# Performance work log

Measured on AMD Instinct MI355X. Metric: run time of the kernel, lower is better.

The kernel has to match this reference:

```python
import jax, jax.numpy as jnp
import numpy as np

B, T, C = 2, 2048, 1024
H, D = 16, 64          # n_heads, head_dim
E, K, HD = 8, 2, 1536  # num_experts, active_experts, expert hidden (int(1.5*C))
EPS = 1e-6


def setup_inputs() -> dict:
    key = jax.random.key(0)
    ks = jax.random.split(key, 13)
    s = 0.02
    return {
        "x": jax.random.normal(ks[0], (B, T, C), jnp.float32),
        "rope_cos": jax.random.uniform(ks[1], (T, D), jnp.float32),
        "rope_sin": jax.random.uniform(ks[2], (T, D), jnp.float32),
        "attn_norm_w": jnp.ones((C,), jnp.float32),
        "q_w": jax.random.normal(ks[3], (C, C), jnp.float32) * s,
        "k_w": jax.random.normal(ks[4], (C, C), jnp.float32) * s,
        "v_w": jax.random.normal(ks[5], (C, C), jnp.float32) * s,
        "o_w": jax.random.normal(ks[6], (C, C), jnp.float32) * s,
        "ffn_norm_w": jnp.ones((C,), jnp.float32),
        "router_w": jax.random.normal(ks[7], (E, C), jnp.float32) * s,
        "w1": jax.random.normal(ks[8], (E, HD, C), jnp.float32) * s,
        "w2": jax.random.normal(ks[9], (E, C, HD), jnp.float32) * s,
        "w3": jax.random.normal(ks[10], (E, HD, C), jnp.float32) * s,
    }


def rmsnorm(x, w):
    var = jnp.mean(x * x, axis=-1, keepdims=True)
    return w * x * jax.lax.rsqrt(var + EPS)


def apply_rope(x, cos, sin):
    # x: [B, T, H, D]; cos/sin: [T, D]
    cos = cos[None, :, None, :]
    sin = sin[None, :, None, :]
    d = x.shape[-1] // 2
    x1, x2 = x[..., :d], x[..., d:]
    rotated = jnp.concatenate([-x2, x1], axis=-1)
    return x * cos + rotated * sin


def reference(x, rope_cos, rope_sin, attn_norm_w, q_w, k_w, v_w, o_w,
              ffn_norm_w, router_w, w1, w2, w3):
    b, t, c = x.shape
    h = rmsnorm(x, attn_norm_w)
    q = (h @ q_w.T).reshape(b, t, H, D)
    k = (h @ k_w.T).reshape(b, t, H, D)
    v = (h @ v_w.T).reshape(b, t, H, D)
    q = apply_rope(q, rope_cos[:t], rope_sin[:t]).transpose(0, 2, 1, 3)  # [B,H,T,D]
    k = apply_rope(k, rope_cos[:t], rope_sin[:t]).transpose(0, 2, 1, 3)
    v = v.transpose(0, 2, 1, 3)
    scores = jnp.einsum('bhqd,bhkd->bhqk', q, k) / jnp.sqrt(jnp.asarray(D, q.dtype))
    causal = jnp.tril(jnp.ones((t, t), bool))
    scores = jnp.where(causal, scores, -jnp.inf)
    attn = jax.nn.softmax(scores, axis=-1)
    y = jnp.einsum('bhqk,bhkd->bhqd', attn, v)
    y = y.transpose(0, 2, 1, 3).reshape(b, t, c)
    x = x + y @ o_w.T

    # Sparse MoE (top-K routing, per-expert SwiGLU, weighted combine)
    hn = rmsnorm(x, ffn_norm_w)
    flat = hn.reshape(-1, c)                                # [N, C]
    logits = flat @ router_w.T                              # [N, E]
    wk, idx = jax.lax.top_k(logits, K)                      # [N, K]
    wk = jax.nn.softmax(wk, axis=-1)
    # combined per-expert gate: [N, E] (zero for unrouted experts)
    gate = jnp.sum((idx[..., None] == jnp.arange(E)) * wk[..., None], axis=1)
    out = jnp.zeros_like(flat)
    for e in range(E):
        g = jax.nn.silu(flat @ w1[e].T) * (flat @ w3[e].T)  # [N, HD]
        out = out + gate[:, e:e + 1] * (g @ w2[e].T)
    return x + out.reshape(b, t, c)
```

## Files before the change

### kernel.cpp

```cpp
#include <hip/hip_runtime.h>
#include <hip/hip_bf16.h>
#include <math.h>

#define Bq 2
#define Tq 2048
#define Cq 1024
#define Hq 16
#define Dq 64
#define Eq 8
#define HDq 1536
#define NTOK (Bq*Tq)

typedef unsigned short u16;
typedef _Float16 f16;
typedef __bf16 bf16x8 __attribute__((ext_vector_type(8)));
typedef _Float16 f16x8 __attribute__((ext_vector_type(8)));
typedef float f32x4v __attribute__((ext_vector_type(4)));

#define MB(x) ((size_t)(x) * 262144)

__device__ __forceinline__ float silu_f(float a) {
    return a / (1.0f + __expf(-a));
}
__device__ __forceinline__ u16 f2bf(float f) {
    union { float f; unsigned u; } a; a.f = f;
    unsigned r = a.u + 0x7fffu + ((a.u >> 16) & 1u);
    return (u16)(r >> 16);
}
__device__ __forceinline__ u16 f16bits(f16 h) {
    union { f16 f; u16 u; } a; a.f = h; return a.u;
}

__device__ __forceinline__ void stage16(const void* g, void* l) {
    __builtin_amdgcn_global_load_lds(
        (const __attribute__((address_space(1))) unsigned int*)g,
        (__attribute__((address_space(3))) unsigned int*)l, 16, 0, 0);
}

__global__ __launch_bounds__(256) void rmsnorm_split_k(const float* __restrict__ x,
                                                       const float* __restrict__ w,
                                                       u16* __restrict__ hh,
                                                       u16* __restrict__ hl) {
    int row = blockIdx.x;
    int tid = threadIdx.x;
    const float* xr = x + (size_t)row * Cq;
    float4 v = *(const float4*)(xr + tid * 4);
    float ss = v.x*v.x + v.y*v.y + v.z*v.z + v.w*v.w;
    #pragma unroll
    for (int off = 32; off; off >>= 1) ss += __shfl_xor(ss, off);
    __shared__ float red[4];
    if ((tid & 63) == 0) red[tid >> 6] = ss;
    __syncthreads();
    float tot = red[0] + red[1] + red[2] + red[3];
    float scale = rsqrtf(tot * (1.0f / (float)Cq) + 1e-6f);
    float4 wv = *(const float4*)(w + tid * 4);
    float o[4] = { v.x*wv.x*scale, v.y*wv.y*scale, v.z*wv.z*scale, v.w*wv.w*scale };
    ushort4 oh, ol;
    u16* ph = (u16*)&oh; u16* pl = (u16*)&ol;
    #pragma unroll
    for (int i = 0; i < 4; i++) {
        f16 hi = (f16)o[i]; f16 lo = (f16)(o[i] - (float)hi);
        ph[i] = f16bits(hi); pl[i] = f16bits(lo);
    }
    *(ushort4*)(hh + (size_t)row * Cq + tid * 4) = oh;
    *(ushort4*)(hl + (size_t)row * Cq + tid * 4) = ol;
}

__global__ __launch_bounds__(256) void rmsnorm2_k(const float* __restrict__ x,
                                                  const float* __restrict__ w,
                                                  float* __restrict__ hn,
                                                  u16* __restrict__ hnb) {
    int row = blockIdx.x;
    int tid = threadIdx.x;
    const float* xr = x + (size_t)row * Cq;
    float4 v = *(const float4*)(xr + tid * 4);
    float ss = v.x*v.x + v.y*v.y + v.z*v.z + v.w*v.w;
    #pragma unroll
    for (int off = 32; off; off >>= 1) ss += __shfl_xor(ss, off);
    __shared__ float red[4];
    if ((tid & 63) == 0) red[tid >> 6] = ss;
    __syncthreads();
    float tot = red[0] + red[1] + red[2] + red[3];
    float scale = rsqrtf(tot * (1.0f / (float)Cq) + 1e-6f);
    float4 wv = *(const float4*)(w + tid * 4);
    float4 o = make_float4(v.x*wv.x*scale, v.y*wv.y*scale, v.z*wv.z*scale, v.w*wv.w*scale);
    *(float4*)(hn + (size_t)row * Cq + tid * 4) = o;
    ushort4 ob = make_ushort4(f2bf(o.x), f2bf(o.y), f2bf(o.z), f2bf(o.w));
    *(ushort4*)(hnb + (size_t)row * Cq + tid * 4) = ob;
}

__global__ __launch_bounds__(256) void wconv_k(const float* __restrict__ w1,
                                               const float* __restrict__ w3,
                                               const float* __restrict__ w2,
                                               u16* __restrict__ w1b,
                                               u16* __restrict__ w3b,
                                               u16* __restrict__ w2b) {
    int a = blockIdx.y;
    const float* src = (a == 0) ? w1 : ((a == 1) ? w3 : w2);
    u16* dst = (a == 0) ? w1b : ((a == 1) ? w3b : w2b);
    size_t i = ((size_t)blockIdx.x * 256 + threadIdx.x) * 8;
    float4 f0 = *(const float4*)(src + i);
    float4 f1 = *(const float4*)(src + i + 4);
    ushort4 o0 = make_ushort4(f2bf(f0.x), f2bf(f0.y), f2bf(f0.z), f2bf(f0.w));
    ushort4 o1 = make_ushort4(f2bf(f1.x), f2bf(f1.y), f2bf(f1.z), f2bf(f1.w));
    *(ushort4*)(dst + i)     = o0;
    *(ushort4*)(dst + i + 4) = o1;
}

__global__ __launch_bounds__(256) void wsplit_k(const float* __restrict__ qw,
                                                const float* __restrict__ kw,
                                                const float* __restrict__ vw,
                                                const float* __restrict__ ow,
                                                u16* __restrict__ qhp, u16* __restrict__ qlp,
                                                u16* __restrict__ khp, u16* __restrict__ klp,
                                                u16* __restrict__ vhp, u16* __restrict__ vlp,
                                                u16* __restrict__ ohp, u16* __restrict__ olp) {
    int a = blockIdx.y;
    const float* src = (a == 0) ? qw : ((a == 1) ? kw : ((a == 2) ? vw : ow));
    u16* dh = (a == 0) ? qhp : ((a == 1) ? khp : ((a == 2) ? vhp : ohp));
    u16* dl = (a == 0) ? qlp : ((a == 1) ? klp : ((a == 2) ? vlp : olp));
    size_t i = ((size_t)blockIdx.x * 256 + threadIdx.x) * 8;
    float f[8];
    *(float4*)&f[0] = *(const float4*)(src + i);
    *(float4*)&f[4] = *(const float4*)(src + i + 4);
    u16 oh[8], ol[8];
    #pragma unroll
    for (int j = 0; j < 8; j++) {
        f16 hi = (f16)f[j]; f16 lo = (f16)(f[j] - (float)hi);
        oh[j] = f16bits(hi); ol[j] = f16bits(lo);
    }
    *(uint4*)(dh + i) = *(uint4*)oh;
    *(uint4*)(dl + i) = *(uint4*)ol;
}

__global__ __launch_bounds__(256, 3) void gemm_fused(const u16* __restrict__ Ahg,
                                                     const u16* __restrict__ Alg,
                                                     const float* __restrict__ Wq,
                                                     const float* __restrict__ Wk,
                                                     const float* __restrict__ Wv,
                                                     u16* __restrict__ qh_o,
                                                     u16* __restrict__ ql_o,
                                                     u16* __restrict__ kh_o,
                                                     u16* __restrict__ kl_o,
                                                     float* __restrict__ vf_o,
                                                     const float* __restrict__ cosb,
                                                     const float* __restrict__ sinb,
                                                     const float* __restrict__ aux,
                                                     float* __restrict__ outf,
                                                     int kind) {
    __shared__ u16 AhS[2][128*32], AlS[2][128*32], BhS[128*32], BlS[128*32];
    int tid = threadIdx.x;
    int wave = tid >> 6, lane = tid & 63;
    int wm = wave >> 1, wn = wave & 1;
    int bx = blockIdx.x, by = blockIdx.y;
    int proj, nx;
    const float* W;
    if (kind == 0) {
        proj = bx >> 3; nx = bx & 7;
        W = (proj == 0) ? Wq : ((proj == 1) ? Wk : Wv);
    } else {
        proj = 3; nx = bx; W = Wq;
    }

    int srow = tid >> 2, sch = (tid & 3) * 8;
    const u16* A0 = Ahg + (size_t)(by*128 + srow) * Cq + sch;
    const u16* A1 = A0 + (size_t)64 * Cq;
    const u16* L0 = Alg + (size_t)(by*128 + srow) * Cq + sch;
    const u16* L1 = L0 + (size_t)64 * Cq;
    const float* W0 = W + (size_t)(nx*128 + srow) * Cq + sch;
    const float* W1 = W0 + (size_t)64 * Cq;
    int lo0 = srow*32 + sch, lo1 = lo0 + 2048;

    f32x4v acc[4][4];
    #pragma unroll
    for (int i = 0; i < 4; i++)
        #pragma unroll
        for (int j = 0; j < 4; j++)
            #pragma unroll
            for (int r = 0; r < 4; r++) acc[i][j][r] = 0.0f;

    float wr0[8], wr1[8];
    stage16(A0, &AhS[0][lo0]);
    stage16(A1, &AhS[0][lo1]);
    stage16(L0, &AlS[0][lo0]);
    stage16(L1, &AlS[0][lo1]);
    *(float4*)&wr0[0] = *(const float4*)(W0);
    *(float4*)&wr0[4] = *(const float4*)(W0 + 4);
    *(float4*)&wr1[0] = *(const float4*)(W1);
    *(float4*)&wr1[4] = *(const float4*)(W1 + 4);

    int fr = lane & 15, fk = (lane >> 4) * 8;
    int cur = 0;
    for (int k0 = 0; k0 < Cq; k0 += 32, cur ^= 1) {
        __syncthreads();
        {
            f16x8 bh0, bl0, bh1, bl1;
            #pragma unroll
            for (int i = 0; i < 8; i++) {
                f16 h0 = (f16)wr0[i]; bh0[i] = h0; bl0[i] = (f16)(wr0[i] - (float)h0);
                f16 h1 = (f16)wr1[i]; bh1[i] = h1; bl1[i] = (f16)(wr1[i] - (float)h1);
            }
            *(f16x8*)(void*)&BhS[lo0] = bh0;
            *(f16x8*)(void*)&BlS[lo0] = bl0;
            *(f16x8*)(void*)&BhS[lo1] = bh1;
            *(f16x8*)(void*)&BlS[lo1] = bl1;
        }
        __syncthreads();
        int kn = k0 + 32;
        if (kn < Cq) {
            stage16(A0 + kn, &AhS[cur^1][lo0]);
            stage16(A1 + kn, &AhS[cur^1][lo1]);
            stage16(L0 + kn, &AlS[cur^1][lo0]);
            stage16(L1 + kn, &AlS[cur^1][lo1]);
            *(float4*)&wr0[0] = *(const float4*)(W0 + kn);
            *(float4*)&wr0[4] = *(const float4*)(W0 + kn + 4);
            *(float4*)&wr1[0] = *(const float4*)(W1 + kn);
            *(float4*)&wr1[4] = *(const float4*)(W1 + kn + 4);
        }
        f16x8 ah[4], al[4];
        #pragma unroll
        for (int mi = 0; mi < 4; mi++) {
            ah[mi] = *(const f16x8*)(const void*)&AhS[cur][(wm*64 + mi*16 + fr)*32 + fk];
            al[mi] = *(const f16x8*)(const void*)&AlS[cur][(wm*64 + mi*16 + fr)*32 + fk];
        }
        #pragma unroll
        for (int ni = 0; ni < 4; ni++) {
            f16x8 bhf = *(const f16x8*)(const void*)&BhS[(wn*64 + ni*16 + fr)*32 + fk];
            f16x8 blf = *(const f16x8*)(const void*)&BlS[(wn*64 + ni*16 + fr)*32 + fk];
            #pragma unroll
            for (int mi = 0; mi < 4; mi++) {
                acc[mi][ni] = __builtin_amdgcn_mfma_f32_16x16x32_f16(ah[mi], bhf, acc[mi][ni], 0, 0, 0);
                acc[mi][ni] = __builtin_amdgcn_mfma_f32_16x16x32_f16(ah[mi], blf, acc[mi][ni], 0, 0, 0);
                acc[mi][ni] = __builtin_amdgcn_mfma_f32_16x16x32_f16(al[mi], bhf, acc[mi][ni], 0, 0, 0);
            }
        }
    }

    int cr = (lane >> 4) * 4, cc = lane & 15;
    if (proj < 2) {
        u16* dh = (proj == 0) ? qh_o : kh_o;
        u16* dl = (proj == 0) ? ql_o : kl_o;
        float scale = (proj == 0) ? 0.125f : 1.0f;
        int hd = (nx * 2 + wn) * 64;
        #pragma unroll
        for (int mi = 0; mi < 4; mi++)
            #pragma unroll
            for (int r = 0; r < 4; r++) {
                int row = by*128 + wm*64 + mi*16 + cr + r;
                int t = row & (Tq - 1);
                #pragma unroll
                for (int ni = 0; ni < 2; ni++) {
                    int d0 = ni*16 + cc;
                    float a = acc[mi][ni][r];
                    float b = acc[mi][ni+2][r];
                    float c0 = cosb[t*Dq + d0],      s0 = sinb[t*Dq + d0];
                    float c1 = cosb[t*Dq + d0 + 32], s1 = sinb[t*Dq + d0 + 32];
                    float oa = (a * c0 - b * s0) * scale;
                    float ob = (b * c1 + a * s1) * scale;
                    size_t off = (size_t)row * Cq + hd + d0;
                    f16 ha = (f16)oa;
                    f16 hb = (f16)ob;
                    dh[off]      = f16bits(ha);
                    dl[off]      = f16bits((f16)(oa - (float)ha));
                    dh[off + 32] = f16bits(hb);
                    dl[off + 32] = f16bits((f16)(ob - (float)hb));
                }
            }
    } else if (proj == 2) {
        #pragma unroll
        for (int mi = 0; mi < 4; mi++)
            #pragma unroll
            for (int r = 0; r < 4; r++) {
                int row = by*128 + wm*64 + mi*16 + cr + r;
                #pragma unroll
                for (int ni = 0; ni < 4; ni++)
                    vf_o[(size_t)row * Cq + nx*128 + wn*64 + ni*16 + cc] = acc[mi][ni][r];
            }
    } else {
        #pragma unroll
        for (int mi = 0; mi < 4; mi++)
            #pragma unroll
            for (int r = 0; r < 4; r++) {
                int row = by*128 + wm*64 + mi*16 + cr + r;
                #pragma unroll
                for (int ni = 0; ni < 4; ni++) {
                    size_t off = (size_t)row * Cq + nx*128 + wn*64 + ni*16 + cc;
                    outf[off] = acc[mi][ni][r] + aux[off];
                }
            }
    }
}

__global__ __launch_bounds__(256, 2) void gemm_fused2(const u16* __restrict__ Ahg,
                                                      const u16* __restrict__ Alg,
                                                      const u16* __restrict__ Bh0,
                                                      const u16* __restrict__ Bl0,
                                                      const u16* __restrict__ Bh1,
                                                      const u16* __restrict__ Bl1,
                                                      const u16* __restrict__ Bh2,
                                                      const u16* __restrict__ Bl2,
                                                      u16* __restrict__ qh_o,
                                                      u16* __restrict__ ql_o,
                                                      u16* __restrict__ kh_o,
                                                      u16* __restrict__ kl_o,
                                                      float* __restrict__ vf_o,
                                                      const float* __restrict__ cosb,
                                                      const float* __restrict__ sinb,
                                                      const float* __restrict__ aux,
                                                      float* __restrict__ outf,
                                                      int kind) {
    __shared__ u16 AhS[2][128*32], AlS[2][128*32], BhS[2][128*32], BlS[2][128*32];
    int tid = threadIdx.x;
    int wave = tid >> 6, lane = tid & 63;
    int wm = wave >> 1, wn = wave & 1;
    int bx = blockIdx.x, by = blockIdx.y;
    int proj, nx;
    const u16 *Bh, *Bl;
    if (kind == 0) {
        proj = bx >> 3; nx = bx & 7;
        Bh = (proj == 0) ? Bh0 : ((proj == 1) ? Bh1 : Bh2);
        Bl = (proj == 0) ? Bl0 : ((proj == 1) ? Bl1 : Bl2);
    } else {
        proj = 3; nx = bx; Bh = Bh0; Bl = Bl0;
    }

    int srow = tid >> 2, sch = (tid & 3) * 8;
    const u16* A0 = Ahg + (size_t)(by*128 + srow) * Cq + sch;
    const u16* A1 = A0 + (size_t)64 * Cq;
    const u16* L0 = Alg + (size_t)(by*128 + srow) * Cq + sch;
    const u16* L1 = L0 + (size_t)64 * Cq;
    const u16* H0 = Bh + (size_t)(nx*128 + srow) * Cq + sch;
    const u16* H1 = H0 + (size_t)64 * Cq;
    const u16* G0 = Bl + (size_t)(nx*128 + srow) * Cq + sch;
    const u16* G1 = G0 + (size_t)64 * Cq;
    int lo0 = srow*32 + sch, lo1 = lo0 + 2048;

    f32x4v acc[4][4];
    #pragma unroll
    for (int i = 0; i < 4; i++)
        #pragma unroll
        for (int j = 0; j < 4; j++)
            #pragma unroll
            for (int r = 0; r < 4; r++) acc[i][j][r] = 0.0f;

    stage16(A0, &AhS[0][lo0]); stage16(A1, &AhS[0][lo1]);
    stage16(L0, &AlS[0][lo0]); stage16(L1, &AlS[0][lo1]);
    stage16(H0, &BhS[0][lo0]); stage16(H1, &BhS[0][lo1]);
    stage16(G0, &BlS[0][lo0]); stage16(G1, &BlS[0][lo1]);

    int fr = lane & 15, fk = (lane >> 4) * 8;
    int cur = 0;
    for (int k0 = 0; k0 < Cq; k0 += 32, cur ^= 1) {
        __syncthreads();
        int kn = k0 + 32;
        if (kn < Cq) {
            stage16(A0 + kn, &AhS[cur^1][lo0]); stage16(A1 + kn, &AhS[cur^1][lo1]);
            stage16(L0 + kn, &AlS[cur^1][lo0]); stage16(L1 + kn, &AlS[cur^1][lo1]);
            stage16(H0 + kn, &BhS[cur^1][lo0]); stage16(H1 + kn, &BhS[cur^1][lo1]);
            stage16(G0 + kn, &BlS[cur^1][lo0]); stage16(G1 + kn, &BlS[cur^1][lo1]);
        }
        f16x8 ah[4], al[4];
        #pragma unroll
        for (int mi = 0; mi < 4; mi++) {
            ah[mi] = *(const f16x8*)(const void*)&AhS[cur][(wm*64 + mi*16 + fr)*32 + fk];
            al[mi] = *(const f16x8*)(const void*)&AlS[cur][(wm*64 + mi*16 + fr)*32 + fk];
        }
        #pragma unroll
        for (int ni = 0; ni < 4; ni++) {
            f16x8 bhf = *(const f16x8*)(const void*)&BhS[cur][(wn*64 + ni*16 + fr)*32 + fk];
            f16x8 blf = *(const f16x8*)(const void*)&BlS[cur][(wn*64 + ni*16 + fr)*32 + fk];
            #pragma unroll
            for (int mi = 0; mi < 4; mi++) {
                acc[mi][ni] = __builtin_amdgcn_mfma_f32_16x16x32_f16(ah[mi], bhf, acc[mi][ni], 0, 0, 0);
                acc[mi][ni] = __builtin_amdgcn_mfma_f32_16x16x32_f16(ah[mi], blf, acc[mi][ni], 0, 0, 0);
                acc[mi][ni] = __builtin_amdgcn_mfma_f32_16x16x32_f16(al[mi], bhf, acc[mi][ni], 0, 0, 0);
            }
        }
    }

    int cr = (lane >> 4) * 4, cc = lane & 15;
    if (proj < 2) {
        u16* dh = (proj == 0) ? qh_o : kh_o;
        u16* dl = (proj == 0) ? ql_o : kl_o;
        float scale = (proj == 0) ? 0.125f : 1.0f;
        int hd = (nx * 2 + wn) * 64;
        #pragma unroll
        for (int mi = 0; mi < 4; mi++)
            #pragma unroll
            for (int r = 0; r < 4; r++) {
                int row = by*128 + wm*64 + mi*16 + cr + r;
                int t = row & (Tq - 1);
                #pragma unroll
                for (int ni = 0; ni < 2; ni++) {
                    int d0 = ni*16 + cc;
                    float a = acc[mi][ni][r];
                    float b = acc[mi][ni+2][r];
                    float c0 = cosb[t*Dq + d0],      s0 = sinb[t*Dq + d0];
                    float c1 = cosb[t*Dq + d0 + 32], s1 = sinb[t*Dq + d0 + 32];
                    float oa = (a * c0 - b * s0) * scale;
                    float ob = (b * c1 + a * s1) * scale;
                    size_t off = (size_t)row * Cq + hd + d0;
                    f16 ha = (f16)oa;
                    f16 hb = (f16)ob;
                    dh[off]      = f16bits(ha);
                    dl[off]      = f16bits((f16)(oa - (float)ha));
                    dh[off + 32] = f16bits(hb);
                    dl[off + 32] = f16bits((f16)(ob - (float)hb));
                }
            }
    } else if (proj == 2) {
        #pragma unroll
        for (int mi = 0; mi < 4; mi++)
            #pragma unroll
            for (int r = 0; r < 4; r++) {
                int row = by*128 + wm*64 + mi*16 + cr + r;
                #pragma unroll
                for (int ni = 0; ni < 4; ni++)
                    vf_o[(size_t)row * Cq + nx*128 + wn*64 + ni*16 + cc] = acc[mi][ni][r];
            }
    } else {
        #pragma unroll
        for (int mi = 0; mi < 4; mi++)
            #pragma unroll
            for (int r = 0; r < 4; r++) {
                int row = by*128 + wm*64 + mi*16 + cr + r;
                #pragma unroll
                for (int ni = 0; ni < 4; ni++) {
                    size_t off = (size_t)row * Cq + nx*128 + wn*64 + ni*16 + cc;
                    outf[off] = acc[mi][ni][r] + aux[off];
                }
            }
    }
}

__global__ __launch_bounds__(256) void vtrans_k(const float* __restrict__ v,
                                                u16* __restrict__ vth,
                                                u16* __restrict__ vtl) {
    __shared__ u16 Th[64 * 72];
    __shared__ u16 Tl[64 * 72];
    int tc = blockIdx.x;
    int bh = blockIdx.y;
    int b = bh >> 4, h = bh & 15;
    int tid = threadIdx.x;
    int tr = tid >> 2;
    int dc = (tid & 3) * 16;
    size_t gin = ((size_t)(b * Tq + tc * 64 + tr)) * Cq + h * Dq + dc;
    #pragma unroll
    for (int i = 0; i < 16; i += 4) {
        float4 f = *(const float4*)(v + gin + i);
        float fv[4] = {f.x, f.y, f.z, f.w};
        #pragma unroll
        for (int j = 0; j < 4; j++) {
            f16 hi = (f16)fv[j];
            f16 lo = (f16)(fv[j] - (float)hi);
            Th[(dc + i + j) * 72 + tr] = f16bits(hi);
            Tl[(dc + i + j) * 72 + tr] = f16bits(lo);
        }
    }
    __syncthreads();
    int dr = tid >> 2;
    int cc = (tid & 3) * 16;
    size_t gout = ((size_t)(bh * 64 + dr)) * Tq + tc * 64 + cc;
    *(uint4*)(vth + gout)     = *(uint4*)(Th + dr * 72 + cc);
    *(uint4*)(vth + gout + 8) = *(uint4*)(Th + dr * 72 + cc + 8);
    *(uint4*)(vtl + gout)     = *(uint4*)(Tl + dr * 72 + cc);
    *(uint4*)(vtl + gout + 8) = *(uint4*)(Tl + dr * 72 + cc + 8);
}

#define AST 72
__global__ __launch_bounds__(256, 2) void attn_f16(const u16* __restrict__ qh_g,
                                                   const u16* __restrict__ ql_g,
                                                   const u16* __restrict__ kh_g,
                                                   const u16* __restrict__ kl_g,
                                                   const u16* __restrict__ vth_g,
                                                   const u16* __restrict__ vtl_g,
                                                   u16* __restrict__ yh_g,
                                                   u16* __restrict__ yl_g) {
    __shared__ u16 Qh[64*AST], Ql[64*AST];
    __shared__ u16 Kh[64*AST], Kl[64*AST];
    __shared__ u16 Vh[64*AST], Vl[64*AST];
    __shared__ u16 Ph[64*AST], Pl[64*AST];

    int id = blockIdx.x;
    int bh = id & 31;
    int j  = id >> 5;
    int b = bh >> 4, h = bh & 15;
    int tid = threadIdx.x;
    int wv = tid >> 6, lane = tid & 63;
    int fr = lane & 15, fg = lane >> 4;
    int sr = tid >> 2, sc = (tid & 3) * 16;
    int aoff = (wv * 16 + fr) * AST + fg * 8;

    uint4 rkh0, rkh1, rkl0, rkl1, rvh0, rvh1, rvl0, rvl1;
    auto ldkv = [&](int kt) {
        size_t kg = ((size_t)(b * Tq + kt * 64 + sr)) * Cq + h * Dq + sc;
        size_t vg = ((size_t)(bh * 64 + sr)) * Tq + kt * 64 + sc;
        rkh0 = *(const uint4*)(kh_g + kg);  rkh1 = *(const uint4*)(kh_g + kg + 8);
        rkl0 = *(const uint4*)(kl_g + kg);  rkl1 = *(const uint4*)(kl_g + kg + 8);
        rvh0 = *(const uint4*)(vth_g + vg); rvh1 = *(const uint4*)(vth_g + vg + 8);
        rvl0 = *(const uint4*)(vtl_g + vg); rvl1 = *(const uint4*)(vtl_g + vg + 8);
    };

    #pragma unroll
    for (int pass = 0; pass < 2; pass++) {
        int qt = pass == 0 ? (31 - j) : j;

        __syncthreads();
        {
            size_t g = ((size_t)(b * Tq + qt * 64 + sr)) * Cq + h * Dq + sc;
            *(uint4*)(Qh + sr*AST + sc)     = *(const uint4*)(qh_g + g);
            *(uint4*)(Qh + sr*AST + sc + 8) = *(const uint4*)(qh_g + g + 8);
            *(uint4*)(Ql + sr*AST + sc)     = *(const uint4*)(ql_g + g);
            *(uint4*)(Ql + sr*AST + sc + 8) = *(const uint4*)(ql_g + g + 8);
        }
        ldkv(0);

        f16x8 aqh0 = *(const f16x8*)(const void*)(Qh + aoff);
        f16x8 aqh1 = *(const f16x8*)(const void*)(Qh + aoff + 32);
        f16x8 aql0 = *(const f16x8*)(const void*)(Ql + aoff);
        f16x8 aql1 = *(const f16x8*)(const void*)(Ql + aoff + 32);

        f32x4v acc_o[4];
        float m_i[4], l_i[4];
        #pragma unroll
        for (int i = 0; i < 4; i++) {
            m_i[i] = -1e30f; l_i[i] = 0.0f;
            #pragma unroll
            for (int r = 0; r < 4; r++) acc_o[i][r] = 0.0f;
        }

        for (int kt = 0; kt <= qt; kt++) {
            __syncthreads();
            *(uint4*)(Kh + sr*AST + sc)     = rkh0;
            *(uint4*)(Kh + sr*AST + sc + 8) = rkh1;
            *(uint4*)(Kl + sr*AST + sc)     = rkl0;
            *(uint4*)(Kl + sr*AST + sc + 8) = rkl1;
            *(uint4*)(Vh + sr*AST + sc)     = rvh0;
            *(uint4*)(Vh + sr*AST + sc + 8) = rvh1;
            *(uint4*)(Vl + sr*AST + sc)     = rvl0;
            *(uint4*)(Vl + sr*AST + sc + 8) = rvl1;
            __syncthreads();
            if (kt < qt) ldkv(kt + 1);

            f32x4v s[4];
            __builtin_amdgcn_s_setprio(1);
            #pragma unroll
            for (int ni = 0; ni < 4; ni++) {
                int boff = (ni * 16 + fr) * AST + fg * 8;
                f16x8 kh0 = *(const f16x8*)(const void*)(Kh + boff);
                f16x8 kh1 = *(const f16x8*)(const void*)(Kh + boff + 32);
                f16x8 kl0 = *(const f16x8*)(const void*)(Kl + boff);
                f16x8 kl1 = *(const f16x8*)(const void*)(Kl + boff + 32);
                f32x4v t;
                #pragma unroll
                for (int r = 0; r < 4; r++) t[r] = 0.0f;
                t = __builtin_amdgcn_mfma_f32_16x16x32_f16(aqh0, kh0, t, 0, 0, 0);
                t = __builtin_amdgcn_mfma_f32_16x16x32_f16(aqh1, kh1, t, 0, 0, 0);
                t = __builtin_amdgcn_mfma_f32_16x16x32_f16(aqh0, kl0, t, 0, 0, 0);
                t = __builtin_amdgcn_mfma_f32_16x16x32_f16(aqh1, kl1, t, 0, 0, 0);
                t = __builtin_amdgcn_mfma_f32_16x16x32_f16(aql0, kh0, t, 0, 0, 0);
                t = __builtin_amdgcn_mfma_f32_16x16x32_f16(aql1, kh1, t, 0, 0, 0);
                s[ni] = t;
            }
            __builtin_amdgcn_s_setprio(0);

            if (kt == qt) {
                #pragma unroll
                for (int ni = 0; ni < 4; ni++) {
                    int col = ni * 16 + fr;
                    #pragma unroll
                    for (int r = 0; r < 4; r++) {
                        int row = wv * 16 + fg * 4 + r;
                        if (col > row) s[ni][r] = -1e30f;
                    }
                }
            }

            float p[4][4];
            #pragma unroll
            for (int r = 0; r < 4; r++) {
                float mx = fmaxf(fmaxf(s[0][r], s[1][r]), fmaxf(s[2][r], s[3][r]));
                #pragma unroll
                for (int off = 1; off < 16; off <<= 1)
                    mx = fmaxf(mx, __shfl_xor(mx, off, 16));
                float mn = fmaxf(m_i[r], mx);
                float rs = 0.0f;
                #pragma unroll
                for (int ni = 0; ni < 4; ni++) {
                    p[ni][r] = __expf(s[ni][r] - mn);
                    rs += p[ni][r];
                }
                #pragma unroll
                for (int off = 1; off < 16; off <<= 1)
                    rs += __shfl_xor(rs, off, 16);
                float alpha = __expf(m_i[r] - mn);
                l_i[r] = l_i[r] * alpha + rs;
                m_i[r] = mn;
                #pragma unroll
                for (int ni = 0; ni < 4; ni++) acc_o[ni][r] *= alpha;
            }

            #pragma unroll
            for (int ni = 0; ni < 4; ni++) {
                #pragma unroll
                for (int r = 0; r < 4; r++) {
                    int off = (wv * 16 + fg * 4 + r) * AST + ni * 16 + fr;
                    f16 ph = (f16)p[ni][r];
                    f16 pl = (f16)(p[ni][r] - (float)ph);
                    Ph[off] = f16bits(ph);
                    Pl[off] = f16bits(pl);
                }
            }

            f16x8 aph0 = *(const f16x8*)(const void*)(Ph + aoff);
            f16x8 aph1 = *(const f16x8*)(const void*)(Ph + aoff + 32);
            f16x8 apl0 = *(const f16x8*)(const void*)(Pl + aoff);
            f16x8 apl1 = *(const f16x8*)(const void*)(Pl + aoff + 32);
            __builtin_amdgcn_s_setprio(1);
            #pragma unroll
            for (int ni = 0; ni < 4; ni++) {
                int boff = (ni * 16 + fr) * AST + fg * 8;
                f16x8 vh0 = *(const f16x8*)(const void*)(Vh + boff);
                f16x8 vh1 = *(const f16x8*)(const void*)(Vh + boff + 32);
                f16x8 vl0 = *(const f16x8*)(const void*)(Vl + boff);
                f16x8 vl1 = *(const f16x8*)(const void*)(Vl + boff + 32);
                f32x4v t = acc_o[ni];
                t = __builtin_amdgcn_mfma_f32_16x16x32_f16(aph0, vh0, t, 0, 0, 0);
                t = __builtin_amdgcn_mfma_f32_16x16x32_f16(aph1, vh1, t, 0, 0, 0);
                t = __builtin_amdgcn_mfma_f32_16x16x32_f16(aph0, vl0, t, 0, 0, 0);
                t = __builtin_amdgcn_mfma_f32_16x16x32_f16(aph1, vl1, t, 0, 0, 0);
                t = __builtin_amdgcn_mfma_f32_16x16x32_f16(apl0, vh0, t, 0, 0, 0);
                t = __builtin_amdgcn_mfma_f32_16x16x32_f16(apl1, vh1, t, 0, 0, 0);
                acc_o[ni] = t;
            }
            __builtin_amdgcn_s_setprio(0);
        }

        #pragma unroll
        for (int r = 0; r < 4; r++) {
            float inv = 1.0f / l_i[r];
            int row = qt * 64 + wv * 16 + fg * 4 + r;
            size_t base = ((size_t)(b * Tq + row)) * Cq + h * Dq + fr;
            #pragma unroll
            for (int ni = 0; ni < 4; ni++) {
                float yv = acc_o[ni][r] * inv;
                f16 hi = (f16)yv;
                f16 lo = (f16)(yv - (float)hi);
                yh_g[base + ni * 16] = f16bits(hi);
                yl_g[base + ni * 16] = f16bits(lo);
            }
        }
    }
}

__global__ void zero_k(int* cnt) {
    if (threadIdx.x < Eq) cnt[threadIdx.x] = 0;
}

__global__ __launch_bounds__(64) void router_k(const float* __restrict__ hn,
                                               const float* __restrict__ rw,
                                               int* __restrict__ cnt,
                                               int* __restrict__ idxl,
                                               float* __restrict__ gvl) {
    int tkn = blockIdx.x;
    int lane = threadIdx.x;
    float acc[Eq] = {};
    for (int it = 0; it < Cq / 64; it++) {
        float hv = hn[(size_t)tkn * Cq + it * 64 + lane];
        #pragma unroll
        for (int e = 0; e < Eq; e++)
            acc[e] = fmaf(hv, rw[e * Cq + it * 64 + lane], acc[e]);
    }
    #pragma unroll
    for (int e = 0; e < Eq; e++) {
        #pragma unroll
        for (int off = 32; off; off >>= 1) acc[e] += __shfl_xor(acc[e], off);
    }
    int i0 = 0;
    #pragma unroll
    for (int e = 1; e < Eq; e++) if (acc[e] > acc[i0]) i0 = e;
    int i1 = (i0 == 0) ? 1 : 0;
    #pragma unroll
    for (int e = 0; e < Eq; e++)
        if (e != i0 && acc[e] > acc[i1]) i1 = e;
    float p1 = __expf(acc[i1] - acc[i0]);
    float g0 = 1.0f / (1.0f + p1);
    float g1 = p1 / (1.0f + p1);
    if (lane == 0) {
        int p0 = atomicAdd(&cnt[i0], 1);
        idxl[i0 * NTOK + p0] = tkn;
        gvl[i0 * NTOK + p0] = g0;
        int p1i = atomicAdd(&cnt[i1], 1);
        idxl[i1 * NTOK + p1i] = tkn;
        gvl[i1 * NTOK + p1i] = g1;
    }
}

__global__ void setup_k(const int* __restrict__ cnt, int* __restrict__ seg,
                        int* __restrict__ texp, int* __restrict__ ttot) {
    if (threadIdx.x == 0) {
        int base = 0;
        for (int e = 0; e < Eq; e++) {
            seg[e] = base * 128;
            int t = (cnt[e] + 127) >> 7;
            for (int i = 0; i < t; i++) texp[base + i] = e;
            base += t;
        }
        *ttot = base;
    }
}

__global__ __launch_bounds__(256, 2) void moe_w13b(const u16* __restrict__ hnb,
                                                   const u16* __restrict__ w1b,
                                                   const u16* __restrict__ w3b,
                                                   u16* __restrict__ gbuf,
                                                   const int* __restrict__ cnt,
                                                   const int* __restrict__ seg,
                                                   const int* __restrict__ texp,
                                                   const int* __restrict__ ttot,
                                                   const int* __restrict__ idxl) {
    int by = blockIdx.y;
    if (by >= *ttot) return;
    int e = texp[by];
    const u16* w1e = w1b + (size_t)e * HDq * Cq;
    const u16* w3e = w3b + (size_t)e * HDq * Cq;
    int cnte = cnt[e], sege = seg[e];
    const int* idxe = idxl + e * NTOK;

    __shared__ u16 As[2][128*32], B1S[2][128*32], B3S[2][128*32];
    int tid = threadIdx.x;
    int wave = tid >> 6, lane = tid & 63;
    int wm = wave >> 1, wn = wave & 1;
    int bx = blockIdx.x;
    int srow = tid >> 2, sch = (tid & 3) * 8;

    int r0 = by*128 + srow, r1 = r0 + 64;
    int li0 = r0 - sege, li1 = r1 - sege;
    int tok0 = idxe[li0 < cnte ? li0 : 0];
    int tok1 = idxe[li1 < cnte ? li1 : 0];
    const u16* A0 = hnb + (size_t)tok0 * Cq + sch;
    const u16* A1 = hnb + (size_t)tok1 * Cq + sch;
    const u16* W10 = w1e + (size_t)(bx*128 + srow) * Cq + sch;
    const u16* W11 = W10 + (size_t)64 * Cq;
    const u16* W30 = w3e + (size_t)(bx*128 + srow) * Cq + sch;
    const u16* W31 = W30 + (size_t)64 * Cq;
    int lo0 = srow*32 + sch, lo1 = lo0 + 2048;

    f32x4v acc1[4][4], acc3[4][4];
    #pragma unroll
    for (int i = 0; i < 4; i++)
        #pragma unroll
        for (int j = 0; j < 4; j++)
            #pragma unroll
            for (int r = 0; r < 4; r++) { acc1[i][j][r] = 0.0f; acc3[i][j][r] = 0.0f; }

    stage16(A0,  &As[0][lo0]);  stage16(A1,  &As[0][lo1]);
    stage16(W10, &B1S[0][lo0]); stage16(W11, &B1S[0][lo1]);
    stage16(W30, &B3S[0][lo0]); stage16(W31, &B3S[0][lo1]);

    int fr = lane & 15, fk = (lane >> 4) * 8;
    int cur = 0;
    for (int k0 = 0; k0 < Cq; k0 += 32, cur ^= 1) {
        __syncthreads();
        int kn = k0 + 32;
        if (kn < Cq) {
            stage16(A0 + kn,  &As[cur^1][lo0]);  stage16(A1 + kn,  &As[cur^1][lo1]);
            stage16(W10 + kn, &B1S[cur^1][lo0]); stage16(W11 + kn, &B1S[cur^1][lo1]);
            stage16(W30 + kn, &B3S[cur^1][lo0]); stage16(W31 + kn, &B3S[cur^1][lo1]);
        }
        bf16x8 af[4];
        #pragma unroll
        for (int mi = 0; mi < 4; mi++)
            af[mi] = *(const bf16x8*)&As[cur][(wm*64 + mi*16 + fr) * 32 + fk];
        #pragma unroll
        for (int ni = 0; ni < 4; ni++) {
            bf16x8 b1f = *(const bf16x8*)&B1S[cur][(wn*64 + ni*16 + fr) * 32 + fk];
            bf16x8 b3f = *(const bf16x8*)&B3S[cur][(wn*64 + ni*16 + fr) * 32 + fk];
            #pragma unroll
            for (int mi = 0; mi < 4; mi++) {
                acc1[mi][ni] = __builtin_amdgcn_mfma_f32_16x16x32_bf16(af[mi], b1f, acc1[mi][ni], 0, 0, 0);
                acc3[mi][ni] = __builtin_amdgcn_mfma_f32_16x16x32_bf16(af[mi], b3f, acc3[mi][ni], 0, 0, 0);
            }
        }
    }

    int cr = (lane >> 4) * 4, cc = lane & 15;
    #pragma unroll
    for (int mi = 0; mi < 4; mi++)
        #pragma unroll
        for (int ni = 0; ni < 4; ni++)
            #pragma unroll
            for (int r = 0; r < 4; r++) {
                int row = by*128 + wm*64 + mi*16 + cr + r;
                int col = bx*128 + wn*64 + ni*16 + cc;
                gbuf[(size_t)row * HDq + col] = f2bf(silu_f(acc1[mi][ni][r]) * acc3[mi][ni][r]);
            }
}

__global__ __launch_bounds__(256, 3) void moe_w2b_k(const u16* __restrict__ gbuf,
                                                    const u16* __restrict__ w2b,
                                                    float* __restrict__ out,
                                                    const int* __restrict__ cnt,
                                                    const int* __restrict__ seg,
                                                    const int* __restrict__ texp,
                                                    const int* __restrict__ ttot,
                                                    const int* __restrict__ idxl,
                                                    const float* __restrict__ gvl) {
    int by = blockIdx.y;
    if (by >= *ttot) return;
    int e = texp[by];
    const u16* w2e = w2b + (size_t)e * Cq * HDq;
    int cnte = cnt[e], sege = seg[e];
    const int* idxe = idxl + e * NTOK;
    const float* gve = gvl + e * NTOK;

    __shared__ u16 As[2][128*32], Bs[2][128*32];
    int tid = threadIdx.x;
    int wave = tid >> 6, lane = tid & 63;
    int wm = wave >> 1, wn = wave & 1;
    int bx = blockIdx.x;
    int srow = tid >> 2, sch = (tid & 3) * 8;

    const u16* A0 = gbuf + (size_t)(by*128 + srow) * HDq + sch;
    const u16* A1 = A0 + (size_t)64 * HDq;
    const u16* W0 = w2e + (size_t)(bx*128 + srow) * HDq + sch;
    const u16* W1 = W0 + (size_t)64 * HDq;
    int lo0 = srow*32 + sch, lo1 = lo0 + 2048;

    f32x4v acc[4][4];
    #pragma unroll
    for (int i = 0; i < 4; i++)
        #pragma unroll
        for (int j = 0; j < 4; j++)
            #pragma unroll
            for (int r = 0; r < 4; r++) acc[i][j][r] = 0.0f;

    stage16(A0, &As[0][lo0]); stage16(A1, &As[0][lo1]);
    stage16(W0, &Bs[0][lo0]); stage16(W1, &Bs[0][lo1]);

    int fr = lane & 15, fk = (lane >> 4) * 8;
    int cur = 0;
    for (int k0 = 0; k0 < HDq; k0 += 32, cur ^= 1) {
        __syncthreads();
        int kn = k0 + 32;
        if (kn < HDq) {
            stage16(A0 + kn, &As[cur^1][lo0]); stage16(A1 + kn, &As[cur^1][lo1]);
            stage16(W0 + kn, &Bs[cur^1][lo0]); stage16(W1 + kn, &Bs[cur^1][lo1]);
        }
        bf16x8 af[4];
        #pragma unroll
        for (int mi = 0; mi < 4; mi++)
            af[mi] = *(const bf16x8*)&As[cur][(wm*64 + mi*16 + fr) * 32 + fk];
        #pragma unroll
        for (int ni = 0; ni < 4; ni++) {
            bf16x8 bf_ = *(const bf16x8*)&Bs[cur][(wn*64 + ni*16 + fr) * 32 + fk];
            #pragma unroll
            for (int mi = 0; mi < 4; mi++)
                acc[mi][ni] = __builtin_amdgcn_mfma_f32_16x16x32_bf16(af[mi], bf_, acc[mi][ni], 0, 0, 0);
        }
    }

    int cr = (lane >> 4) * 4, cc = lane & 15;
    #pragma unroll
    for (int mi = 0; mi < 4; mi++)
        #pragma unroll
        for (int r = 0; r < 4; r++) {
            int row = by*128 + wm*64 + mi*16 + cr + r;
            int local = row - sege;
            if (local < cnte) {
                int token = idxe[local];
                float g = gve[local];
                #pragma unroll
                for (int ni = 0; ni < 4; ni++) {
                    int col = bx*128 + wn*64 + ni*16 + cc;
                    atomicAdd(&out[(size_t)token * Cq + col], g * acc[mi][ni][r]);
                }
            }
        }
}

__global__ __launch_bounds__(256, 2) void moe_w13(const u16* __restrict__ hnb,
                                                  const float* __restrict__ w1,
                                                  const float* __restrict__ w3,
                                                  u16* __restrict__ gbuf,
                                                  const int* __restrict__ cnt,
                                                  const int* __restrict__ seg,
                                                  const int* __restrict__ texp,
                                                  const int* __restrict__ ttot,
                                                  const int* __restrict__ idxl) {
    int by = blockIdx.y;
    if (by >= *ttot) return;
    int e = texp[by];
    const float* w1e = w1 + (size_t)e * HDq * Cq;
    const float* w3e = w3 + (size_t)e * HDq * Cq;
    int cnte = cnt[e], sege = seg[e];
    const int* idxe = idxl + e * NTOK;

    __shared__ u16 As[2][128*32], B1S[128*32], B3S[128*32];
    int tid = threadIdx.x;
    int wave = tid >> 6, lane = tid & 63;
    int wm = wave >> 1, wn = wave & 1;
    int bx = blockIdx.x;
    int srow = tid >> 2, sch = (tid & 3) * 8;

    int r0 = by*128 + srow, r1 = r0 + 64;
    int li0 = r0 - sege, li1 = r1 - sege;
    int tok0 = idxe[li0 < cnte ? li0 : 0];
    int tok1 = idxe[li1 < cnte ? li1 : 0];
    const u16* A0 = hnb + (size_t)tok0 * Cq + sch;
    const u16* A1 = hnb + (size_t)tok1 * Cq + sch;
    const float* W10 = w1e + (size_t)(bx*128 + srow) * Cq + sch;
    const float* W11 = W10 + (size_t)64 * Cq;
    const float* W30 = w3e + (size_t)(bx*128 + srow) * Cq + sch;
    const float* W31 = W30 + (size_t)64 * Cq;
    int lo0 = srow*32 + sch, lo1 = lo0 + 2048;

    f32x4v acc1[4][4], acc3[4][4];
    #pragma unroll
    for (int i = 0; i < 4; i++)
        #pragma unroll
        for (int j = 0; j < 4; j++)
            #pragma unroll
            for (int r = 0; r < 4; r++) { acc1[i][j][r] = 0.0f; acc3[i][j][r] = 0.0f; }

    float x1a[8], x1b[8], x3a[8], x3b[8];
    stage16(A0, &As[0][lo0]);
    stage16(A1, &As[0][lo1]);
    *(float4*)&x1a[0] = *(const float4*)(W10);
    *(float4*)&x1a[4] = *(const float4*)(W10 + 4);
    *(float4*)&x1b[0] = *(const float4*)(W11);
    *(float4*)&x1b[4] = *(const float4*)(W11 + 4);
    *(float4*)&x3a[0] = *(const float4*)(W30);
    *(float4*)&x3a[4] = *(const float4*)(W30 + 4);
    *(float4*)&x3b[0] = *(const float4*)(W31);
    *(float4*)&x3b[4] = *(const float4*)(W31 + 4);

    int fr = lane & 15, fk = (lane >> 4) * 8;
    int cur = 0;
    for (int k0 = 0; k0 < Cq; k0 += 32, cur ^= 1) {
        __syncthreads();
        {
            u16 t0[8], t1[8], t2[8], t3[8];
            #pragma unroll
// ... 265 lines not shown
```

Measured before the change: 726.9 us.

## Compute transposed scores in attention to keep P in registers

The attention kernel now computes S^T by swapping the MFMA operands, so each lane holds one query row's scores. Softmax statistics then need only two cross-lane shuffles instead of a 16-lane reduction per row. The P tile is redistributed into the A-operand layout with register shuffles instead of a round trip through shared memory, and Q fragments are loaded straight from global memory. Dropping the Q and P shared buffers frees LDS, and launch bounds are raised to 3 blocks per CU. The cost is many shuffle instructions and possibly more register pressure under the tighter occupancy bound.

```diff
diff --git a/kernel.cpp b/kernel.cpp
--- a/kernel.cpp
+++ b/kernel.cpp
@@ -12,6 +12,7 @@
 #define NTOK (Bq*Tq)
 
 typedef unsigned short u16;
+typedef unsigned int u32;
 typedef _Float16 f16;
 typedef __bf16 bf16x8 __attribute__((ext_vector_type(8)));
 typedef _Float16 f16x8 __attribute__((ext_vector_type(8)));
@@ -468,7 +469,7 @@
 }
 
 #define AST 72
-__global__ __launch_bounds__(256, 2) void attn_f16(const u16* __restrict__ qh_g,
+__global__ __launch_bounds__(256, 3) void attn_f16(const u16* __restrict__ qh_g,
                                                    const u16* __restrict__ ql_g,
                                                    const u16* __restrict__ kh_g,
                                                    const u16* __restrict__ kl_g,
@@ -476,10 +477,8 @@
                                                    const u16* __restrict__ vtl_g,
                                                    u16* __restrict__ yh_g,
                                                    u16* __restrict__ yl_g) {
-    __shared__ u16 Qh[64*AST], Ql[64*AST];
     __shared__ u16 Kh[64*AST], Kl[64*AST];
     __shared__ u16 Vh[64*AST], Vl[64*AST];
-    __shared__ u16 Ph[64*AST], Pl[64*AST];
 
     int id = blockIdx.x;
     int bh = id & 31;
@@ -489,7 +488,10 @@
     int wv = tid >> 6, lane = tid & 63;
     int fr = lane & 15, fg = lane >> 4;
     int sr = tid >> 2, sc = (tid & 3) * 16;
-    int aoff = (wv * 16 + fr) * AST + fg * 8;
+
+    int idx0 = fr + ((fg & 1) << 5);
+    int idx1 = idx0 + 16;
+    int hiw = fg >> 1;
 
     uint4 rkh0, rkh1, rkl0, rkl1, rvh0, rvh1, rvl0, rvl1;
     auto ldkv = [&](int kt) {
@@ -505,29 +507,19 @@
     for (int pass = 0; pass < 2; pass++) {
         int qt = pass == 0 ? (31 - j) : j;
 
-        __syncthreads();
-        {
-            size_t g = ((size_t)(b * Tq + qt * 64 + sr)) * Cq + h * Dq + sc;
-            *(uint4*)(Qh + sr*AST + sc)     = *(const uint4*)(qh_g + g);
-            *(uint4*)(Qh + sr*AST + sc + 8) = *(const uint4*)(qh_g + g + 8);
-            *(uint4*)(Ql + sr*AST + sc)     = *(const uint4*)(ql_g + g);
-            *(uint4*)(Ql + sr*AST + sc + 8) = *(const uint4*)(ql_g + g + 8);
-        }
+        size_t qg = ((size_t)(b * Tq + qt * 64 + wv * 16 + fr)) * Cq + h * Dq + fg * 8;
+        f16x8 aqh0 = *(const f16x8*)(const void*)(qh_g + qg);
+        f16x8 aqh1 = *(const f16x8*)(const void*)(qh_g + qg + 32);
+        f16x8 aql0 = *(const f16x8*)(const void*)(ql_g + qg);
+        f16x8 aql1 = *(const f16x8*)(const void*)(ql_g + qg + 32);
         ldkv(0);
 
-        f16x8 aqh0 = *(const f16x8*)(const void*)(Qh + aoff);
-        f16x8 aqh1 = *(const f16x8*)(const void*)(Qh + aoff + 32);
-        f16x8 aql0 = *(const f16x8*)(const void*)(Ql + aoff);
-        f16x8 aql1 = *(const f16x8*)(const void*)(Ql + aoff + 32);
-
         f32x4v acc_o[4];
-        float m_i[4], l_i[4];
-        #pragma unroll
-        for (int i = 0; i < 4; i++) {
-            m_i[i] = -1e30f; l_i[i] = 0.0f;
+        float m_i = -1e30f, l_i = 0.0f;
+        #pragma unroll
+        for (int i = 0; i < 4; i++)
             #pragma unroll
             for (int r = 0; r < 4; r++) acc_o[i][r] = 0.0f;
-        }
 
         for (int kt = 0; kt <= qt; kt++) {
             __syncthreads();
@@ -554,68 +546,107 @@
                 f32x4v t;
                 #pragma unroll
                 for (int r = 0; r < 4; r++) t[r] = 0.0f;
-                t = __builtin_amdgcn_mfma_f32_16x16x32_f16(aqh0, kh0, t, 0, 0, 0);
-                t = __builtin_amdgcn_mfma_f32_16x16x32_f16(aqh1, kh1, t, 0, 0, 0);
-                t = __builtin_amdgcn_mfma_f32_16x16x32_f16(aqh0, kl0, t, 0, 0, 0);
-                t = __builtin_amdgcn_mfma_f32_16x16x32_f16(aqh1, kl1, t, 0, 0, 0);
-                t = __builtin_amdgcn_mfma_f32_16x16x32_f16(aql0, kh0, t, 0, 0, 0);
-                t = __builtin_amdgcn_mfma_f32_16x16x32_f16(aql1, kh1, t, 0, 0, 0);
+                t = __builtin_amdgcn_mfma_f32_16x16x32_f16(kh0, aqh0, t, 0, 0, 0);
+                t = __builtin_amdgcn_mfma_f32_16x16x32_f16(kh1, aqh1, t, 0, 0, 0);
+                t = __builtin_amdgcn_mfma_f32_16x16x32_f16(kl0, aqh0, t, 0, 0, 0);
+                t = __builtin_amdgcn_mfma_f32_16x16x32_f16(kl1, aqh1, t, 0, 0, 0);
+                t = __builtin_amdgcn_mfma_f32_16x16x32_f16(kh0, aql0, t, 0, 0, 0);
+                t = __builtin_amdgcn_mfma_f32_16x16x32_f16(kh1, aql1, t, 0, 0, 0);
                 s[ni] = t;
             }
             __builtin_amdgcn_s_setprio(0);
 
             if (kt == qt) {
+                int qloc = wv * 16 + fr;
                 #pragma unroll
                 for (int ni = 0; ni < 4; ni++) {
-                    int col = ni * 16 + fr;
                     #pragma unroll
                     for (int r = 0; r < 4; r++) {
-                        int row = wv * 16 + fg * 4 + r;
-                        if (col > row) s[ni][r] = -1e30f;
+                        if (ni * 16 + fg * 4 + r > qloc) s[ni][r] = -1e30f;
                     }
                 }
             }
 
+            float mx = s[0][0];
+            #pragma unroll
+            for (int ni = 0; ni < 4; ni++)
+                #pragma unroll
+                for (int r = 0; r < 4; r++) mx = fmaxf(mx, s[ni][r]);
+            mx = fmaxf(mx, __shfl_xor(mx, 16));
+            mx = fmaxf(mx, __shfl_xor(mx, 32));
+            float mn = fmaxf(m_i, mx);
             float p[4][4];
-            #pragma unroll
-            for (int r = 0; r < 4; r++) {
-                float mx = fmaxf(fmaxf(s[0][r], s[1][r]), fmaxf(s[2][r], s[3][r]));
-                #pragma unroll
-                for (int off = 1; off < 16; off <<= 1)
-                    mx = fmaxf(mx, __shfl_xor(mx, off, 16));
-                float mn = fmaxf(m_i[r], mx);
-                float rs = 0.0f;
-                #pragma unroll
-                for (int ni = 0; ni < 4; ni++) {
+            float rs = 0.0f;
+            #pragma unroll
+            for (int ni = 0; ni < 4; ni++)
+                #pragma unroll
+                for (int r = 0; r < 4; r++) {
                     p[ni][r] = __expf(s[ni][r] - mn);
                     rs += p[ni][r];
                 }
-                #pragma unroll
-                for (int off = 1; off < 16; off <<= 1)
-                    rs += __shfl_xor(rs, off, 16);
-                float alpha = __expf(m_i[r] - mn);
-                l_i[r] = l_i[r] * alpha + rs;
-                m_i[r] = mn;
-                #pragma unroll
-                for (int ni = 0; ni < 4; ni++) acc_o[ni][r] *= alpha;
-            }
-
+            rs += __shfl_xor(rs, 16);
+            rs += __shfl_xor(rs, 32);
+            float alpha = __expf(m_i - mn);
+            l_i = l_i * alpha + rs;
+            m_i = mn;
+
+            #pragma unroll
+            for (int r = 0; r < 4; r++) {
+                float ar = __shfl(alpha, 20 * fg + r);
+                #pragma unroll
+                for (int ni = 0; ni < 4; ni++) acc_o[ni][r] *= ar;
+            }
+
+            u32 wh[8], wl[8];
             #pragma unroll
             for (int ni = 0; ni < 4; ni++) {
                 #pragma unroll
-                for (int r = 0; r < 4; r++) {
-                    int off = (wv * 16 + fg * 4 + r) * AST + ni * 16 + fr;
-                    f16 ph = (f16)p[ni][r];
-                    f16 pl = (f16)(p[ni][r] - (float)ph);
-                    Ph[off] = f16bits(ph);
-                    Pl[off] = f16bits(pl);
+                for (int pr = 0; pr < 2; pr++) {
+                    float pa = p[ni][pr*2], pb = p[ni][pr*2 + 1];
+                    f16 ha = (f16)pa, hb = (f16)pb;
+                    wh[ni*2 + pr] = (u32)f16bits(ha) | ((u32)f16bits(hb) << 16);
+                    f16 la = (f16)(pa - (float)ha), lb = (f16)(pb - (float)hb);
+                    wl[ni*2 + pr] = (u32)f16bits(la) | ((u32)f16bits(lb) << 16);
                 }
             }
 
-            f16x8 aph0 = *(const f16x8*)(const void*)(Ph + aoff);
-            f16x8 aph1 = *(const f16x8*)(const void*)(Ph + aoff + 32);
-            f16x8 apl0 = *(const f16x8*)(const void*)(Pl + aoff);
-            f16x8 apl1 = *(const f16x8*)(const void*)(Pl + aoff + 32);
+            union { u32 u[4]; f16x8 v; } fh0, fh1, fl0, fl1;
+            {
+                u32 a, c;
+                a = __shfl((int)wh[0], idx0); c = __shfl((int)wh[2], idx0);
+                fh0.u[0] = hiw ? c : a;
+                a = __shfl((int)wh[1], idx0); c = __shfl((int)wh[3], idx0);
+                fh0.u[1] = hiw ? c : a;
+                a = __shfl((int)wh[0], idx1); c = __shfl((int)wh[2], idx1);
+                fh0.u[2] = hiw ? c : a;
+                a = __shfl((int)wh[1], idx1); c = __shfl((int)wh[3], idx1);
+                fh0.u[3] = hiw ? c : a;
+                a = __shfl((int)wh[4], idx0); c = __shfl((int)wh[6], idx0);
+                fh1.u[0] = hiw ? c : a;
+                a = __shfl((int)wh[5], idx0); c = __shfl((int)wh[7], idx0);
+                fh1.u[1] = hiw ? c : a;
+                a = __shfl((int)wh[4], idx1); c = __shfl((int)wh[6], idx1);
+                fh1.u[2] = hiw ? c : a;
+                a = __shfl((int)wh[5], idx1); c = __shfl((int)wh[7], idx1);
+                fh1.u[3] = hiw ? c : a;
+                a = __shfl((int)wl[0], idx0); c = __shfl((int)wl[2], idx0);
+                fl0.u[0] = hiw ? c : a;
+                a = __shfl((int)wl[1], idx0); c = __shfl((int)wl[3], idx0);
+                fl0.u[1] = hiw ? c : a;
+                a = __shfl((int)wl[0], idx1); c = __shfl((int)wl[2], idx1);
+                fl0.u[2] = hiw ? c : a;
+                a = __shfl((int)wl[1], idx1); c = __shfl((int)wl[3], idx1);
+                fl0.u[3] = hiw ? c : a;
+                a = __shfl((int)wl[4], idx0); c = __shfl((int)wl[6], idx0);
+                fl1.u[0] = hiw ? c : a;
+                a = __shfl((int)wl[5], idx0); c = __shfl((int)wl[7], idx0);
+                fl1.u[1] = hiw ? c : a;
+                a = __shfl((int)wl[4], idx1); c = __shfl((int)wl[6], idx1);
+                fl1.u[2] = hiw ? c : a;
+                a = __shfl((int)wl[5], idx1); c = __shfl((int)wl[7], idx1);
+                fl1.u[3] = hiw ? c : a;
+            }
+
             __builtin_amdgcn_s_setprio(1);
             #pragma unroll
             for (int ni = 0; ni < 4; ni++) {
@@ -625,12 +656,12 @@
                 f16x8 vl0 = *(const f16x8*)(const void*)(Vl + boff);
                 f16x8 vl1 = *(const f16x8*)(const void*)(Vl + boff + 32);
                 f32x4v t = acc_o[ni];
-                t = __builtin_amdgcn_mfma_f32_16x16x32_f16(aph0, vh0, t, 0, 0, 0);
-                t = __builtin_amdgcn_mfma_f32_16x16x32_f16(aph1, vh1, t, 0, 0, 0);
-                t = __builtin_amdgcn_mfma_f32_16x16x32_f16(aph0, vl0, t, 0, 0, 0);
-                t = __builtin_amdgcn_mfma_f32_16x16x32_f16(aph1, vl1, t, 0, 0, 0);
-                t = __builtin_amdgcn_mfma_f32_16x16x32_f16(apl0, vh0, t, 0, 0, 0);
-                t = __builtin_amdgcn_mfma_f32_16x16x32_f16(apl1, vh1, t, 0, 0, 0);
+                t = __builtin_amdgcn_mfma_f32_16x16x32_f16(fh0.v, vh0, t, 0, 0, 0);
+                t = __builtin_amdgcn_mfma_f32_16x16x32_f16(fh1.v, vh1, t, 0, 0, 0);
+                t = __builtin_amdgcn_mfma_f32_16x16x32_f16(fh0.v, vl0, t, 0, 0, 0);
+                t = __builtin_amdgcn_mfma_f32_16x16x32_f16(fh1.v, vl1, t, 0, 0, 0);
+                t = __builtin_amdgcn_mfma_f32_16x16x32_f16(fl0.v, vh0, t, 0, 0, 0);
+                t = __builtin_amdgcn_mfma_f32_16x16x32_f16(fl1.v, vh1, t, 0, 0, 0);
                 acc_o[ni] = t;
             }
             __builtin_amdgcn_s_setprio(0);
@@ -638,7 +669,8 @@
 
         #pragma unroll
         for (int r = 0; r < 4; r++) {
-            float inv = 1.0f / l_i[r];
+            float lq = __shfl(l_i, 20 * fg + r);
+            float inv = 1.0f / lq;
             int row = qt * 64 + wv * 16 + fg * 4 + r;
             size_t base = ((size_t)(b * Tq + row)) * Cq + h * Dq + fr;
             #pragma unroll
```

New measurement: 717.9 us. Within noise of the previous version (-1.2%).
